# Kernel tuning notes

Hardware: AMD Instinct MI355X
Metric: run time of the kernel (lower is better)

The kernel has to match this reference:

```python
import jax, jax.numpy as jnp
import numpy as np


def _conv(x, w, b, stride, pad):
    y = jax.lax.conv_general_dilated(x, w, (stride, stride), [(pad, pad), (pad, pad)],
                                     dimension_numbers=('NCHW', 'OIHW', 'NCHW'))
    return y + b[None, :, None, None]


def _maxpool(x, k, s, pad=0):
    # PyTorch MaxPool2d pads with -inf
    return jax.lax.reduce_window(x, -jnp.inf, jax.lax.max,
                                 (1, 1, k, k), (1, 1, s, s),
                                 [(0, 0), (0, 0), (pad, pad), (pad, pad)])


def _squash(s):
    # squash along last axis: ||s||^2/(1+||s||^2) * s/||s||
    sq = jnp.sum(s * s, axis=-1, keepdims=True)
    return (sq / (1.0 + sq)) * s / jnp.sqrt(sq + 1e-8)


def setup_inputs() -> dict:
    key = jax.random.key(0)
    ks = jax.random.split(key, 16)

    def w(k, shape, fan_in):
        return jax.random.normal(k, shape, jnp.float32) / np.float32(np.sqrt(fan_in))

    inp = {}
    inp['x'] = jax.random.normal(ks[0], (64, 3, 227, 227), jnp.float32)
    # AlexNet conv stack
    inp['w1'] = w(ks[1], (96, 3, 11, 11), 3 * 11 * 11);   inp['b1'] = jnp.zeros((96,), jnp.float32)
    inp['w2'] = w(ks[2], (256, 96, 5, 5), 96 * 5 * 5);    inp['b2'] = jnp.zeros((256,), jnp.float32)
    inp['w3'] = w(ks[3], (384, 256, 3, 3), 256 * 3 * 3);  inp['b3'] = jnp.zeros((384,), jnp.float32)
    inp['w4'] = w(ks[4], (384, 384, 3, 3), 384 * 3 * 3);  inp['b4'] = jnp.zeros((384,), jnp.float32)
    inp['w5'] = w(ks[5], (256, 384, 3, 3), 384 * 3 * 3);  inp['b5'] = jnp.zeros((256,), jnp.float32)
    # PrimaryCaps: 32 caps * 8 dims = 256 output channels
    inp['pc_w'] = w(ks[6], (256, 256, 3, 3), 256 * 3 * 3); inp['pc_b'] = jnp.zeros((256,), jnp.float32)
    # DenseCapsule transform weights [out_caps, in_caps, out_dim, in_dim]
    inp['caps_W'] = 0.01 * jax.random.normal(ks[7], (101, 1152, 16, 8), jnp.float32)
    # MLP head (torch Linear convention: [out, in])
    inp['fc1_w'] = w(ks[8], (4096, 101 * 16), 101 * 16);  inp['fc1_b'] = jnp.zeros((4096,), jnp.float32)
    inp['fc2_w'] = w(ks[9], (4096, 4096), 4096);          inp['fc2_b'] = jnp.zeros((4096,), jnp.float32)
    inp['fc3_w'] = w(ks[10], (101, 4096), 4096);          inp['fc3_b'] = jnp.zeros((101,), jnp.float32)
    return inp


def reference(x, w1, b1, w2, b2, w3, b3, w4, b4, w5, b5,
              pc_w, pc_b, caps_W, fc1_w, fc1_b, fc2_w, fc2_b, fc3_w, fc3_b):
    # --- AlexNet conv stack ---
    h = jax.nn.relu(_conv(x, w1, b1, 4, 0))   # [B,96,55,55]
    h = _maxpool(h, 3, 2, 0)                   # [B,96,27,27]
    h = jax.nn.relu(_conv(h, w2, b2, 1, 2))    # [B,256,27,27]
    h = _maxpool(h, 3, 2, 1)                   # [B,256,14,14]
    h = jax.nn.relu(_conv(h, w3, b3, 1, 1))
    h = jax.nn.relu(_conv(h, w4, b4, 1, 1))
    h = jax.nn.relu(_conv(h, w5, b5, 1, 1))    # [B,256,14,14]
    h = _maxpool(h, 3, 2, 0)                   # [B,256,6,6]

    # --- PrimaryCaps: conv -> reshape to capsules -> squash ---
    p = _conv(h, pc_w, pc_b, 1, 1)             # [B,256,6,6]
    B = p.shape[0]
    u = _squash(p.reshape(B, -1, 8))           # [B,1152,8]

    # --- DenseCapsule dynamic routing (3 iterations) ---
    x_hat = jnp.einsum('jiod,bid->bjio', caps_W, u)   # [B,101,1152,16]
    x_hat_det = jax.lax.stop_gradient(x_hat)
    b_logits = jnp.zeros((B, 101, 1152), x_hat.dtype)
    routings = 3
    for r in range(routings):
        c = jax.nn.softmax(b_logits, axis=1)  # coupling coeffs over out caps
        if r == routings - 1:
            v = _squash(jnp.einsum('bji,bjio->bjo', c, x_hat))
        else:
            v = _squash(jnp.einsum('bji,bjio->bjo', c, x_hat_det))
            b_logits = b_logits + jnp.einsum('bjo,bjio->bji', v, x_hat_det)

    # --- MLP head (dropout in eval mode = identity) ---
    f = v.reshape(B, -1)                       # [B,1616]
    f = jax.nn.relu(f @ fc1_w.T + fc1_b)
    f = jax.nn.relu(f @ fc2_w.T + fc2_b)
    return f @ fc3_w.T + fc3_b                 # [B,101]
```

## Files before the change

kernel.cpp:

```cpp
#include <hip/hip_runtime.h>
#include <math.h>


#define BATCH 64
#define NJ 101
#define NI 1152
#define BJ (BATCH * NJ)
#define IC 64
#define NIC (NI / IC)
#define LDW 132

static inline int ceil_div(int a, int b) { return (a + b - 1) / b; }

typedef __attribute__((ext_vector_type(8))) short short8;
typedef __attribute__((ext_vector_type(4))) float f32x4;

__device__ __forceinline__ unsigned short f2bf(float f) {
    unsigned u = __float_as_uint(f);
    u += 0x7FFFu + ((u >> 16) & 1u);
    return (unsigned short)(u >> 16);
}
__device__ __forceinline__ float bf2f(unsigned short h) {
    return __uint_as_float(((unsigned)h) << 16);
}
__device__ __forceinline__ unsigned packsplit(float v) {
    unsigned short h = f2bf(v);
    unsigned short l = f2bf(v - bf2f(h));
    return ((unsigned)h << 16) | l;
}

__global__ void split_w(const float* __restrict__ w, unsigned short* __restrict__ hi,
                        unsigned short* __restrict__ lo, int Ktot, int Kp, int total) {
    int idx = blockIdx.x * 256 + threadIdx.x;
    if (idx >= total) return;
    int co = idx / Kp, kp = idx - co * Kp;
    float v = (kp < Ktot) ? w[(size_t)co * Ktot + kp] : 0.f;
    unsigned short h = f2bf(v);
    hi[idx] = h;
    lo[idx] = f2bf(v - bf2f(h));
}

template<int K, int STRIDE, int PAD, int WOUT, bool RELU, int TCO,
         bool INPK, bool OUTPK>
__global__ __launch_bounds__(256, 4) void conv_mfma(
        const void* __restrict__ inv, const float* __restrict__ wgt,
        const unsigned short* __restrict__ whi, const unsigned short* __restrict__ wlo,
        const float* __restrict__ bias, void* __restrict__ outv,
        int CIN, int COUT, int WIN, int Kp) {
    constexpr int KK  = K * K;
    constexpr int NSP = WOUT * WOUT;
    constexpr int LDH = 40;
    constexpr int NT  = TCO / 32;
    __shared__ unsigned short Ahs[TCO * LDH], Als[TCO * LDH];
    __shared__ unsigned short Bhs[64 * LDH],  Bls[64 * LDH];

    const int Ktot  = CIN * KK;
    const int WINSQ = WIN * WIN;

    const int tid  = threadIdx.x;
    const int px0  = blockIdx.x * 64;
    const int co0  = blockIdx.y * TCO;
    const int wave = tid >> 6;
    const int lane = tid & 63;
    const int ln15 = lane & 15;
    const int kq   = lane >> 4;
    const int coH  = (wave & 1) * (TCO / 2);
    const int pxH  = (wave >> 1) * 32;

    const int bpx = tid & 63;
    int p    = px0 + bpx;
    int bimg = p / NSP;
    int sp   = p - bimg * NSP;
    int ho   = sp / WOUT;
    int wo   = sp - ho * WOUT;
    const int hi0   = ho * STRIDE - PAD;
    const int wi0   = wo * STRIDE - PAD;
    const int bBase = bimg * CIN * WINSQ;

    const int aco = tid >> 3;
    const int ak4 = tid & 7;

    f32x4 acc[NT][2];
#pragma unroll
    for (int ct = 0; ct < NT; ++ct)
#pragma unroll
        for (int pt = 0; pt < 2; ++pt)
            acc[ct][pt] = (f32x4){0.f, 0.f, 0.f, 0.f};

    const int nchunks = (Ktot + 31) / 32;
    for (int c = 0; c < nchunks; ++c) {
        const int k0 = c * 32;
        if (whi) {
#pragma unroll
            for (int it = 0; it < TCO / 32; ++it) {
                int slot = tid + it * 256;
                int co = slot >> 3;
                int k4 = slot & 7;
                int row = (co0 + co) * Kp + k0 + k4 * 4;
                ushort4 h4 = *(const ushort4*)&whi[row];
                ushort4 l4 = *(const ushort4*)&wlo[row];
                *(ushort4*)&Ahs[co * LDH + k4 * 4] = h4;
                *(ushort4*)&Als[co * LDH + k4 * 4] = l4;
            }
        } else {
#pragma unroll
            for (int it = 0; it < TCO / 32; ++it) {
                int slot = tid + it * 256;
                int co = slot >> 3;
                int k4 = slot & 7;
                int k  = k0 + k4 * 4;
                float4 w4 = make_float4(0.f, 0.f, 0.f, 0.f);
                const float* wp = wgt + (size_t)(co0 + co) * Ktot + k;
                if (k + 3 < Ktot) {
                    w4 = *(const float4*)wp;
                } else {
                    if (k + 0 < Ktot) w4.x = wp[0];
                    if (k + 1 < Ktot) w4.y = wp[1];
                    if (k + 2 < Ktot) w4.z = wp[2];
                    if (k + 3 < Ktot) w4.w = wp[3];
                }
                unsigned short h0 = f2bf(w4.x), h1 = f2bf(w4.y),
                               h2 = f2bf(w4.z), h3 = f2bf(w4.w);
                unsigned short l0 = f2bf(w4.x - bf2f(h0)), l1 = f2bf(w4.y - bf2f(h1)),
                               l2 = f2bf(w4.z - bf2f(h2)), l3 = f2bf(w4.w - bf2f(h3));
                *(uint2*)&Ahs[co * LDH + k4 * 4] =
                    make_uint2(h0 | ((unsigned)h1 << 16), h2 | ((unsigned)h3 << 16));
                *(uint2*)&Als[co * LDH + k4 * 4] =
                    make_uint2(l0 | ((unsigned)l1 << 16), l2 | ((unsigned)l3 << 16));
            }
        }
#pragma unroll
        for (int it = 0; it < 4; ++it) {
            int kp = (tid >> 6) + it * 4;
            if (INPK) {
                const unsigned* inp = (const unsigned*)inv;
                unsigned u0 = 0, u1 = 0;
#pragma unroll
                for (int e = 0; e < 2; ++e) {
                    int k = k0 + kp * 2 + e;
                    unsigned v = 0;
                    if (k < Ktot) {
                        int ci = k / KK;
                        int r  = k - ci * KK;
                        int kh = r / K;
                        int kw = r - kh * K;
                        int hh = hi0 + kh;
                        int ww = wi0 + kw;
                        bool ok = true;
                        if (PAD > 0)
                            ok = ((unsigned)hh < (unsigned)WIN) &&
                                 ((unsigned)ww < (unsigned)WIN);
                        if (ok) v = inp[bBase + ci * WINSQ + hh * WIN + ww];
                    }
                    if (e == 0) u0 = v; else u1 = v;
                }
                *(unsigned*)&Bhs[bpx * LDH + kp * 2] = (u0 >> 16) | (u1 & 0xFFFF0000u);
                *(unsigned*)&Bls[bpx * LDH + kp * 2] = (u0 & 0xFFFFu) | (u1 << 16);
            } else {
                const float* inp = (const float*)inv;
                float f0 = 0.f, f1 = 0.f;
#pragma unroll
                for (int e = 0; e < 2; ++e) {
                    int k = k0 + kp * 2 + e;
                    float v = 0.f;
                    if (k < Ktot) {
                        int ci = k / KK;
                        int r  = k - ci * KK;
                        int kh = r / K;
                        int kw = r - kh * K;
                        int hh = hi0 + kh;
                        int ww = wi0 + kw;
                        bool ok = true;
                        if (PAD > 0)
                            ok = ((unsigned)hh < (unsigned)WIN) &&
                                 ((unsigned)ww < (unsigned)WIN);
                        if (ok) v = inp[bBase + ci * WINSQ + hh * WIN + ww];
                    }
                    if (e == 0) f0 = v; else f1 = v;
                }
                unsigned short h0 = f2bf(f0), h1 = f2bf(f1);
                unsigned short l0 = f2bf(f0 - bf2f(h0)), l1 = f2bf(f1 - bf2f(h1));
                *(unsigned*)&Bhs[bpx * LDH + kp * 2] = h0 | ((unsigned)h1 << 16);
                *(unsigned*)&Bls[bpx * LDH + kp * 2] = l0 | ((unsigned)l1 << 16);
            }
        }
        __syncthreads();

        short8 ahf[NT], alf[NT], bhf[2], blf[2];
#pragma unroll
        for (int ct = 0; ct < NT; ++ct) {
            int m = coH + ct * 16 + ln15;
            ahf[ct] = *(const short8*)&Ahs[m * LDH + kq * 8];
            alf[ct] = *(const short8*)&Als[m * LDH + kq * 8];
        }
#pragma unroll
        for (int pt = 0; pt < 2; ++pt) {
            int n = pxH + pt * 16 + ln15;
            bhf[pt] = *(const short8*)&Bhs[n * LDH + kq * 8];
            blf[pt] = *(const short8*)&Bls[n * LDH + kq * 8];
        }
#pragma unroll
        for (int ct = 0; ct < NT; ++ct)
#pragma unroll
            for (int pt = 0; pt < 2; ++pt) {
                acc[ct][pt] = __builtin_amdgcn_mfma_f32_16x16x32_bf16(
                    ahf[ct], bhf[pt], acc[ct][pt], 0, 0, 0);
                acc[ct][pt] = __builtin_amdgcn_mfma_f32_16x16x32_bf16(
                    ahf[ct], blf[pt], acc[ct][pt], 0, 0, 0);
                acc[ct][pt] = __builtin_amdgcn_mfma_f32_16x16x32_bf16(
                    alf[ct], bhf[pt], acc[ct][pt], 0, 0, 0);
            }
        __syncthreads();
    }

    float bv[NT][4];
#pragma unroll
    for (int ct = 0; ct < NT; ++ct)
#pragma unroll
        for (int r = 0; r < 4; ++r)
            bv[ct][r] = bias[co0 + coH + ct * 16 + kq * 4 + r];
#pragma unroll
    for (int pt = 0; pt < 2; ++pt) {
        int pg  = px0 + pxH + pt * 16 + ln15;
        int b2  = pg / NSP;
        int sp2 = pg - b2 * NSP;
#pragma unroll
        for (int ct = 0; ct < NT; ++ct) {
#pragma unroll
            for (int r = 0; r < 4; ++r) {
                int co = co0 + coH + ct * 16 + kq * 4 + r;
                float vv = acc[ct][pt][r] + bv[ct][r];
                if (RELU) vv = fmaxf(vv, 0.f);
                size_t oi = (size_t)(b2 * COUT + co) * NSP + sp2;
                if (OUTPK) ((unsigned*)outv)[oi] = packsplit(vv);
                else       ((float*)outv)[oi] = vv;
            }
        }
    }
}

__global__ void maxpool_pack(const float* __restrict__ in, unsigned* __restrict__ out,
                             int BC, int HIN, int WIN, int HOUT, int WOUT,
                             int KS, int S, int P) {
    int idx = blockIdx.x * blockDim.x + threadIdx.x;
    int total = BC * HOUT * WOUT;
    if (idx >= total) return;
    int wo = idx % WOUT;
    int ho = (idx / WOUT) % HOUT;
    int bc = idx / (WOUT * HOUT);
    int h0 = ho * S - P, w0 = wo * S - P;
    int h1 = h0 + KS, w1 = w0 + KS;
    if (h0 < 0) h0 = 0;
    if (w0 < 0) w0 = 0;
    if (h1 > HIN) h1 = HIN;
    if (w1 > WIN) w1 = WIN;
    const float* base = in + (size_t)bc * HIN * WIN;
    float m = -INFINITY;
    for (int h = h0; h < h1; h++)
        for (int w = w0; w < w1; w++)
            m = fmaxf(m, base[h * WIN + w]);
    out[idx] = packsplit(m);
}

__global__ void squash_u(const float* __restrict__ p, float* __restrict__ u, int ncaps) {
    int idx = blockIdx.x * blockDim.x + threadIdx.x;
    if (idx >= ncaps) return;
    const float4* pp = (const float4*)(p + (size_t)idx * 8);
    float4 a = pp[0], b = pp[1];
    float sq = a.x*a.x + a.y*a.y + a.z*a.z + a.w*a.w
             + b.x*b.x + b.y*b.y + b.z*b.z + b.w*b.w;
    float scale = (sq / (1.f + sq)) / sqrtf(sq + 1e-8f);
    float4* uu = (float4*)(u + (size_t)idx * 8);
    float4 oa, ob;
    oa.x = a.x*scale; oa.y = a.y*scale; oa.z = a.z*scale; oa.w = a.w*scale;
    ob.x = b.x*scale; ob.y = b.y*scale; ob.z = b.z*scale; ob.w = b.w*scale;
    uu[0] = oa; uu[1] = ob;
}

__global__ void softmax_j(const float* __restrict__ blog, float* __restrict__ c,
                          int Bn, int J, int I) {
    int idx = blockIdx.x * blockDim.x + threadIdx.x;
    if (idx >= Bn * I) return;
    int b = idx / I, i = idx - b * I;
    const float* base = blog + (size_t)b * J * I + i;
    float m = -INFINITY;
    for (int j = 0; j < J; j++) m = fmaxf(m, base[(size_t)j * I]);
    float* cb = c + (size_t)b * J * I + i;
    float sum = 0.f;
    for (int j = 0; j < J; j++) {
        float e = expf(base[(size_t)j * I] - m);
        sum += e;
        cb[(size_t)j * I] = e;
    }
    float inv = 1.f / sum;
    for (int j = 0; j < J; j++) cb[(size_t)j * I] *= inv;
}

__device__ __forceinline__ void stage_W(const float* __restrict__ W,
                                        float* __restrict__ wsh,
                                        int j, int i0, int tid) {
    const float4* Wp = (const float4*)(W + ((size_t)j * NI + i0) * 128);
#pragma unroll
    for (int p = 0; p < 8; ++p) {
        int vi  = p * 256 + tid;
        int row = vi >> 5;
        int c4  = vi & 31;
        float4 f = Wp[vi];
        *(float4*)&wsh[row * LDW + c4 * 4] = f;
    }
}

__global__ __launch_bounds__(256) void route_s_w(
        const float* __restrict__ c, const float* __restrict__ u,
        const float* __restrict__ W, float* __restrict__ ppart, int uniform) {
    __shared__ float wsh[IC * LDW];
    const int tid = threadIdx.x;
    const int icb = blockIdx.x;
    const int j   = blockIdx.y;
    const int i0  = icb * IC;

    stage_W(W, wsh, j, i0, tid);
    __syncthreads();

    const int bg = tid >> 4;
    const int iq = tid & 15;
    const float invJ = 1.f / (float)NJ;

    float s[4][16];
#pragma unroll
    for (int bb = 0; bb < 4; ++bb)
#pragma unroll
        for (int o = 0; o < 16; ++o) s[bb][o] = 0.f;

#pragma unroll
    for (int k = 0; k < 4; ++k) {
        int il = iq + 16 * k;
        int ig = i0 + il;
        const float* wr = &wsh[il * LDW];
        float4 ua[4], ub[4];
        float cc[4];
#pragma unroll
        for (int bb = 0; bb < 4; ++bb) {
            int b = bg * 4 + bb;
            const float4* up = (const float4*)(u + ((size_t)b * NI + ig) * 8);
            ua[bb] = up[0];
            ub[bb] = up[1];
            cc[bb] = uniform ? invJ : c[((size_t)b * NJ + j) * NI + ig];
        }
#pragma unroll
        for (int o = 0; o < 16; ++o) {
            float4 w0 = *(const float4*)&wr[o * 8];
            float4 w1 = *(const float4*)&wr[o * 8 + 4];
#pragma unroll
            for (int bb = 0; bb < 4; ++bb) {
                float dot = w0.x*ua[bb].x + w0.y*ua[bb].y + w0.z*ua[bb].z + w0.w*ua[bb].w
                          + w1.x*ub[bb].x + w1.y*ub[bb].y + w1.z*ub[bb].z + w1.w*ub[bb].w;
                s[bb][o] = fmaf(cc[bb], dot, s[bb][o]);
            }
        }
    }

#pragma unroll
    for (int off = 8; off > 0; off >>= 1)
#pragma unroll
        for (int bb = 0; bb < 4; ++bb)
#pragma unroll
            for (int o = 0; o < 16; ++o)
                s[bb][o] += __shfl_down(s[bb][o], off, 16);

    if (iq == 0) {
#pragma unroll
        for (int bb = 0; bb < 4; ++bb) {
            int b = bg * 4 + bb;
            size_t base = ((size_t)icb * BJ + (size_t)b * NJ + j) * 16;
#pragma unroll
            for (int o4 = 0; o4 < 4; ++o4)
                *(float4*)&ppart[base + o4 * 4] =
                    make_float4(s[bb][o4*4+0], s[bb][o4*4+1], s[bb][o4*4+2], s[bb][o4*4+3]);
        }
    }
}

__global__ __launch_bounds__(64) void reduce_squash(
        const float* __restrict__ ppart, float* __restrict__ v) {
    int l = threadIdx.x >> 4;
    int o = threadIdx.x & 15;
    int bj = blockIdx.x * 4 + l;
    float s = 0.f;
    for (int ic = 0; ic < NIC; ic++)
        s += ppart[((size_t)ic * BJ + bj) * 16 + o];
    __shared__ float sarr[4][16];
    sarr[l][o] = s;
    __syncthreads();
    float ssq = 0.f;
#pragma unroll
    for (int k = 0; k < 16; k++) { float t = sarr[l][k]; ssq += t * t; }
    float scale = (ssq / (1.f + ssq)) / sqrtf(ssq + 1e-8f);
    v[(size_t)bj * 16 + o] = s * scale;
}

__global__ __launch_bounds__(256) void route_bupd_w(
        const float* __restrict__ u, const float* __restrict__ W,
        const float* __restrict__ v, float* __restrict__ blog, int accumulate) {
    __shared__ float wsh[IC * LDW];
    const int tid = threadIdx.x;
    const int icb = blockIdx.x;
    const int j   = blockIdx.y;
    const int i0  = icb * IC;

    stage_W(W, wsh, j, i0, tid);
    __syncthreads();

    const int bg = tid >> 4;
    const int iq = tid & 15;

    float vv[4][16];
#pragma unroll
    for (int bb = 0; bb < 4; ++bb) {
        int b = bg * 4 + bb;
        const float4* vp = (const float4*)(v + ((size_t)b * NJ + j) * 16);
#pragma unroll
        for (int o4 = 0; o4 < 4; ++o4) {
            float4 f = vp[o4];
            vv[bb][o4*4+0] = f.x; vv[bb][o4*4+1] = f.y;
            vv[bb][o4*4+2] = f.z; vv[bb][o4*4+3] = f.w;
        }
    }

#pragma unroll
    for (int k = 0; k < 4; ++k) {
        int il = iq + 16 * k;
        int ig = i0 + il;
        const float* wr = &wsh[il * LDW];
        float4 ua[4], ub[4];
#pragma unroll
        for (int bb = 0; bb < 4; ++bb) {
            int b = bg * 4 + bb;
            const float4* up = (const float4*)(u + ((size_t)b * NI + ig) * 8);
            ua[bb] = up[0];
            ub[bb] = up[1];
        }
        float acc[4] = {0.f, 0.f, 0.f, 0.f};
#pragma unroll
        for (int o = 0; o < 16; ++o) {
            float4 w0 = *(const float4*)&wr[o * 8];
            float4 w1 = *(const float4*)&wr[o * 8 + 4];
#pragma unroll
            for (int bb = 0; bb < 4; ++bb) {
                float dot = w0.x*ua[bb].x + w0.y*ua[bb].y + w0.z*ua[bb].z + w0.w*ua[bb].w
                          + w1.x*ub[bb].x + w1.y*ub[bb].y + w1.z*ub[bb].z + w1.w*ub[bb].w;
                acc[bb] = fmaf(vv[bb][o], dot, acc[bb]);
            }
        }
#pragma unroll
        for (int bb = 0; bb < 4; ++bb) {
            int b = bg * 4 + bb;
            size_t idx = ((size_t)b * NJ + j) * NI + ig;
            blog[idx] = accumulate ? (blog[idx] + acc[bb]) : acc[bb];
        }
    }
}

template<bool RELU>
__global__ __launch_bounds__(256, 4) void fc_gemm(
        const float* __restrict__ in, const float* __restrict__ w,
        const float* __restrict__ bias, float* __restrict__ out,
        int M, int N, int Kd) {
    constexpr int KC  = 32;
    constexpr int LDA = 68;
    __shared__ float Ash[KC * LDA];
    __shared__ float Bsh[KC * LDA];

    const int tid = threadIdx.x;
    const int n0 = blockIdx.x * 64;

    const int tn = tid & 15;
    const int tm = tid >> 4;

    float acc[4][4] = {{0.f}};

    for (int k0 = 0; k0 < Kd; k0 += KC) {
#pragma unroll
        for (int it = 0; it < 2; ++it) {
            int idx = tid + it * 256;
            int n   = idx >> 3;
            int k4  = idx & 7;
            int k   = k0 + k4 * 4;
            float4 w4 = make_float4(0.f, 0.f, 0.f, 0.f);
            int ng = n0 + n;
            if (ng < N) {
                const float* wp = w + (size_t)ng * Kd + k;
                if (k + 3 < Kd) {
                    w4 = *(const float4*)wp;
                } else {
                    if (k + 0 < Kd) w4.x = wp[0];
                    if (k + 1 < Kd) w4.y = wp[1];
                    if (k + 2 < Kd) w4.z = wp[2];
                    if (k + 3 < Kd) w4.w = wp[3];
                }
            }
            Ash[(k4 * 4 + 0) * LDA + n] = w4.x;
            Ash[(k4 * 4 + 1) * LDA + n] = w4.y;
            Ash[(k4 * 4 + 2) * LDA + n] = w4.z;
            Ash[(k4 * 4 + 3) * LDA + n] = w4.w;
        }
#pragma unroll
        for (int it = 0; it < 2; ++it) {
            int idx = tid + it * 256;
            int m   = idx >> 3;
            int k4  = idx & 7;
            int k   = k0 + k4 * 4;
            float4 x4 = make_float4(0.f, 0.f, 0.f, 0.f);
            if (m < M) {
                const float* xp = in + (size_t)m * Kd + k;
                if (k + 3 < Kd) {
                    x4 = *(const float4*)xp;
                } else {
                    if (k + 0 < Kd) x4.x = xp[0];
                    if (k + 1 < Kd) x4.y = xp[1];
                    if (k + 2 < Kd) x4.z = xp[2];
                    if (k + 3 < Kd) x4.w = xp[3];
                }
            }
            Bsh[(k4 * 4 + 0) * LDA + m] = x4.x;
            Bsh[(k4 * 4 + 1) * LDA + m] = x4.y;
            Bsh[(k4 * 4 + 2) * LDA + m] = x4.z;
            Bsh[(k4 * 4 + 3) * LDA + m] = x4.w;
        }
        __syncthreads();
#pragma unroll
        for (int kk = 0; kk < KC; ++kk) {
            float4 a4 = *(const float4*)&Ash[kk * LDA + tn * 4];
            float4 b4 = *(const float4*)&Bsh[kk * LDA + tm * 4];
            float av[4] = {a4.x, a4.y, a4.z, a4.w};
            float bv[4] = {b4.x, b4.y, b4.z, b4.w};
#pragma unroll
            for (int i = 0; i < 4; ++i)
#pragma unroll
                for (int j = 0; j < 4; ++j)
                    acc[i][j] = fmaf(av[i], bv[j], acc[i][j]);
        }
        __syncthreads();
    }

#pragma unroll
    for (int i = 0; i < 4; ++i) {
        int ng = n0 + tn * 4 + i;
        if (ng >= N) continue;
        float bs = bias[ng];
#pragma unroll
        for (int j = 0; j < 4; ++j) {
            int m = tm * 4 + j;
            if (m >= M) continue;
            float vv = acc[i][j] + bs;
            if (RELU) vv = fmaxf(vv, 0.f);
            out[(size_t)m * N + ng] = vv;
        }
    }
}

extern "C" void kernel_launch(void* const* d_in, const int* in_sizes, int n_in,
                              void* d_out, int out_size, void* d_ws, size_t ws_size,
                              hipStream_t stream) {
    const float* x     = (const float*)d_in[0];
    const float* w1    = (const float*)d_in[1];
    const float* b1    = (const float*)d_in[2];
    const float* w2    = (const float*)d_in[3];
    const float* b2    = (const float*)d_in[4];
    const float* w3    = (const float*)d_in[5];
    const float* b3    = (const float*)d_in[6];
    const float* w4    = (const float*)d_in[7];
    const float* b4    = (const float*)d_in[8];
    const float* w5    = (const float*)d_in[9];
    const float* b5    = (const float*)d_in[10];
    const float* pc_w  = (const float*)d_in[11];
    const float* pc_b  = (const float*)d_in[12];
    const float* capsW = (const float*)d_in[13];
    const float* fc1_w = (const float*)d_in[14];
    const float* fc1_b = (const float*)d_in[15];
    const float* fc2_w = (const float*)d_in[16];
    const float* fc2_b = (const float*)d_in[17];
    const float* fc3_w = (const float*)d_in[18];
    const float* fc3_b = (const float*)d_in[19];
    float* outp = (float*)d_out;

    char* ws = (char*)d_ws;
    float* A  = (float*)ws;
    float* Bb = (float*)(ws + ((size_t)80 << 20));
    float* Dd = (float*)(ws + ((size_t)100 << 20));
    float* blog  = A;
    float* csm   = A + 7446528;
    float* ppart = A + 2 * 7446528;
    float* vcap = Dd;
    float* f1   = Dd + 131072;
    float* f2   = Dd + 131072 + 262144;

    const size_t WPL_ELEMS = 2ull * (96*384 + 256*2400 + 384*2304 +
                                     384*3456 + 256*3456 + 256*2304);
    const size_t WPL_NEED  = ((size_t)104 << 20) + WPL_ELEMS * 2;
    const bool wsplit = ws_size >= WPL_NEED;
    unsigned short* wp = (unsigned short*)(ws + ((size_t)104 << 20));
    unsigned short *w1h=nullptr,*w1l=nullptr,*w2h=nullptr,*w2l=nullptr,
                   *w3h=nullptr,*w3l=nullptr,*w4h=nullptr,*w4l=nullptr,
                   *w5h=nullptr,*w5l=nullptr,*pch=nullptr,*pcl=nullptr;
    if (wsplit) {
        size_t off = 0;
        auto alloc2 = [&](size_t n, unsigned short** h, unsigned short** l) {
            *h = wp + off; *l = wp + off + n; off += 2 * n;
        };
        alloc2((size_t)96*384,  &w1h, &w1l);
        alloc2((size_t)256*2400, &w2h, &w2l);
        alloc2((size_t)384*2304, &w3h, &w3l);
        alloc2((size_t)384*3456, &w4h, &w4l);
        alloc2((size_t)256*3456, &w5h, &w5l);
        alloc2((size_t)256*2304, &pch, &pcl);
        split_w<<<dim3(ceil_div(96*384, 256)), dim3(256), 0, stream>>>(
            w1, w1h, w1l, 363, 384, 96*384);
        split_w<<<dim3(ceil_div(256*2400, 256)), dim3(256), 0, stream>>>(
            w2, w2h, w2l, 2400, 2400, 256*2400);
        split_w<<<dim3(ceil_div(384*2304, 256)), dim3(256), 0, stream>>>(
            w3, w3h, w3l, 2304, 2304, 384*2304);
        split_w<<<dim3(ceil_div(384*3456, 256)), dim3(256), 0, stream>>>(
            w4, w4h, w4l, 3456, 3456, 384*3456);
        split_w<<<dim3(ceil_div(256*3456, 256)), dim3(256), 0, stream>>>(
            w5, w5h, w5l, 3456, 3456, 256*3456);
        split_w<<<dim3(ceil_div(256*2304, 256)), dim3(256), 0, stream>>>(
            pc_w, pch, pcl, 2304, 2304, 256*2304);
    }

    const int B = BATCH;

    conv_mfma<11, 4, 0, 55, true, 96, false, false>
        <<<dim3(3025, 1), dim3(256), 0, stream>>>(
        x, w1, w1h, w1l, b1, A, 3, 96, 227, 384);
    maxpool_pack<<<dim3(ceil_div(B * 96 * 27 * 27, 256)), dim3(256), 0, stream>>>(
        A, (unsigned*)Bb, B * 96, 55, 55, 27, 27, 3, 2, 0);
    conv_mfma<5, 1, 2, 27, true, 128, true, false>
        <<<dim3(729, 2), dim3(256), 0, stream>>>(
        Bb, w2, w2h, w2l, b2, A, 96, 256, 27, 2400);
    maxpool_pack<<<dim3(ceil_div(B * 256 * 14 * 14, 256)), dim3(256), 0, stream>>>(
        A, (unsigned*)Bb, B * 256, 27, 27, 14, 14, 3, 2, 1);
    conv_mfma<3, 1, 1, 14, true, 128, true, true>
        <<<dim3(196, 3), dim3(256), 0, stream>>>(
        Bb, w3, w3h, w3l, b3, A, 256, 384, 14, 2304);
    conv_mfma<3, 1, 1, 14, true, 128, true, true>
        <<<dim3(196, 3), dim3(256), 0, stream>>>(
        A, w4, w4h, w4l, b4, Bb, 384, 384, 14, 3456);
    conv_mfma<3, 1, 1, 14, true, 128, true, false>
        <<<dim3(196, 2), dim3(256), 0, stream>>>(
        Bb, w5, w5h, w5l, b5, A, 384, 256, 14, 3456);
    maxpool_pack<<<dim3(ceil_div(B * 256 * 6 * 6, 256)), dim3(256), 0, stream>>>(
        A, (unsigned*)Bb, B * 256, 14, 14, 6, 6, 3, 2, 0);
    conv_mfma<3, 1, 1, 6, false, 64, true, false>
        <<<dim3(36, 4), dim3(256), 0, stream>>>(
        Bb, pc_w, pch, pcl, pc_b, A, 256, 256, 6, 2304);
    squash_u<<<dim3(ceil_div(B * 1152, 256)), dim3(256), 0, stream>>>(A, Bb, B * 1152);

    dim3 rgrid(NIC, NJ);
    route_s_w<<<rgrid, dim3(256), 0, stream>>>(csm, Bb, capsW, ppart, 1);
    reduce_squash<<<dim3(BJ / 4), dim3(64), 0, stream>>>(ppart, vcap);
    route_bupd_w<<<rgrid, dim3(256), 0, stream>>>(Bb, capsW, vcap, blog, 0);
    softmax_j<<<dim3(ceil_div(B * NI, 256)), dim3(256), 0, stream>>>(
        blog, csm, B, NJ, NI);
    route_s_w<<<rgrid, dim3(256), 0, stream>>>(csm, Bb, capsW, ppart, 0);
    reduce_squash<<<dim3(BJ / 4), dim3(64), 0, stream>>>(ppart, vcap);
    route_bupd_w<<<rgrid, dim3(256), 0, stream>>>(Bb, capsW, vcap, blog, 1);
    softmax_j<<<dim3(ceil_div(B * NI, 256)), dim3(256), 0, stream>>>(
        blog, csm, B, NJ, NI);
    route_s_w<<<rgrid, dim3(256), 0, stream>>>(csm, Bb, capsW, ppart, 0);
    reduce_squash<<<dim3(BJ / 4), dim3(64), 0, stream>>>(ppart, vcap);

    fc_gemm<true><<<dim3(64), dim3(256), 0, stream>>>(vcap, fc1_w, fc1_b, f1, B, 4096, 1616);
    fc_gemm<true><<<dim3(64), dim3(256), 0, stream>>>(f1, fc2_w, fc2_b, f2, B, 4096, 4096);
    fc_gemm<false><<<dim3(2), dim3(256), 0, stream>>>(f2, fc3_w, fc3_b, outp, B, 101, 4096);
}
```

Baseline: 3.485 ms.

## Prefetch next conv K-chunk into registers and swizzle B tile in LDS

The conv MFMA kernel now gathers the next 32-wide K chunk of weights and im2col inputs into registers while the current chunk's MFMAs run, then stores them to LDS at the top of the next iteration. The B tile columns are XOR-swizzled by pixel index to cut LDS bank conflicts on the stores and on the short8 fragment reads. This hides global-load latency behind compute, at the cost of more registers per thread, which could lower occupancy under the launch bounds of 256 threads and 4 blocks.

```diff
diff --git a/kernel.cpp b/kernel.cpp
--- a/kernel.cpp
+++ b/kernel.cpp
@@ -28,6 +28,7 @@
     unsigned short l = f2bf(v - bf2f(h));
     return ((unsigned)h << 16) | l;
 }
+__device__ __forceinline__ int bswz(int n) { return ((n >> 2) ^ (n >> 4)) & 3; }
 
 __global__ void split_w(const float* __restrict__ w, unsigned short* __restrict__ hi,
                         unsigned short* __restrict__ lo, int Ktot, int Kp, int total) {
@@ -51,6 +52,7 @@
     constexpr int NSP = WOUT * WOUT;
     constexpr int LDH = 40;
     constexpr int NT  = TCO / 32;
+    constexpr int NTA = TCO / 32;
     __shared__ unsigned short Ahs[TCO * LDH], Als[TCO * LDH];
     __shared__ unsigned short Bhs[64 * LDH],  Bls[64 * LDH];
 
@@ -76,6 +78,8 @@
     const int hi0   = ho * STRIDE - PAD;
     const int wi0   = wo * STRIDE - PAD;
     const int bBase = bimg * CIN * WINSQ;
+    const int swzb  = bswz(bpx);
+    const int wq    = tid >> 6;
 
     const int aco = tid >> 3;
     const int ak4 = tid & 7;
@@ -87,24 +91,23 @@
         for (int pt = 0; pt < 2; ++pt)
             acc[ct][pt] = (f32x4){0.f, 0.f, 0.f, 0.f};
 
-    const int nchunks = (Ktot + 31) / 32;
-    for (int c = 0; c < nchunks; ++c) {
-        const int k0 = c * 32;
+    ushort4 pah[NTA], pal[NTA];
+    uint2 pb_cur[4], pb_nxt[4];
+
+    auto gatherA = [&](int k0) {
         if (whi) {
 #pragma unroll
-            for (int it = 0; it < TCO / 32; ++it) {
+            for (int it = 0; it < NTA; ++it) {
                 int slot = tid + it * 256;
                 int co = slot >> 3;
                 int k4 = slot & 7;
                 int row = (co0 + co) * Kp + k0 + k4 * 4;
-                ushort4 h4 = *(const ushort4*)&whi[row];
-                ushort4 l4 = *(const ushort4*)&wlo[row];
-                *(ushort4*)&Ahs[co * LDH + k4 * 4] = h4;
-                *(ushort4*)&Als[co * LDH + k4 * 4] = l4;
+                pah[it] = *(const ushort4*)&whi[row];
+                pal[it] = *(const ushort4*)&wlo[row];
             }
         } else {
 #pragma unroll
-            for (int it = 0; it < TCO / 32; ++it) {
+            for (int it = 0; it < NTA; ++it) {
                 int slot = tid + it * 256;
                 int co = slot >> 3;
                 int k4 = slot & 7;
@@ -121,17 +124,17 @@
                 }
                 unsigned short h0 = f2bf(w4.x), h1 = f2bf(w4.y),
                                h2 = f2bf(w4.z), h3 = f2bf(w4.w);
-                unsigned short l0 = f2bf(w4.x - bf2f(h0)), l1 = f2bf(w4.y - bf2f(h1)),
-                               l2 = f2bf(w4.z - bf2f(h2)), l3 = f2bf(w4.w - bf2f(h3));
-                *(uint2*)&Ahs[co * LDH + k4 * 4] =
-                    make_uint2(h0 | ((unsigned)h1 << 16), h2 | ((unsigned)h3 << 16));
-                *(uint2*)&Als[co * LDH + k4 * 4] =
-                    make_uint2(l0 | ((unsigned)l1 << 16), l2 | ((unsigned)l3 << 16));
-            }
-        }
+                pah[it] = make_ushort4(h0, h1, h2, h3);
+                pal[it] = make_ushort4(f2bf(w4.x - bf2f(h0)), f2bf(w4.y - bf2f(h1)),
+                                       f2bf(w4.z - bf2f(h2)), f2bf(w4.w - bf2f(h3)));
+            }
+        }
+    };
+
+    auto gatherB = [&](int k0, uint2* pb) {
 #pragma unroll
         for (int it = 0; it < 4; ++it) {
-            int kp = (tid >> 6) + it * 4;
+            int kp = wq + it * 4;
             if (INPK) {
                 const unsigned* inp = (const unsigned*)inv;
                 unsigned u0 = 0, u1 = 0;
@@ -154,8 +157,8 @@
                     }
                     if (e == 0) u0 = v; else u1 = v;
                 }
-                *(unsigned*)&Bhs[bpx * LDH + kp * 2] = (u0 >> 16) | (u1 & 0xFFFF0000u);
-                *(unsigned*)&Bls[bpx * LDH + kp * 2] = (u0 & 0xFFFFu) | (u1 << 16);
+                pb[it].x = (u0 >> 16) | (u1 & 0xFFFF0000u);
+                pb[it].y = (u0 & 0xFFFFu) | (u1 << 16);
             } else {
                 const float* inp = (const float*)inv;
                 float f0 = 0.f, f1 = 0.f;
@@ -179,12 +182,38 @@
                     if (e == 0) f0 = v; else f1 = v;
                 }
                 unsigned short h0 = f2bf(f0), h1 = f2bf(f1);
-                unsigned short l0 = f2bf(f0 - bf2f(h0)), l1 = f2bf(f1 - bf2f(h1));
-                *(unsigned*)&Bhs[bpx * LDH + kp * 2] = h0 | ((unsigned)h1 << 16);
-                *(unsigned*)&Bls[bpx * LDH + kp * 2] = l0 | ((unsigned)l1 << 16);
-            }
+                pb[it].x = h0 | ((unsigned)h1 << 16);
+                pb[it].y = (unsigned)f2bf(f0 - bf2f(h0)) |
+                           ((unsigned)f2bf(f1 - bf2f(h1)) << 16);
+            }
+        }
+    };
+
+    const int nchunks = (Ktot + 31) / 32;
+    gatherA(0);
+    gatherB(0, pb_cur);
+
+    for (int c = 0; c < nchunks; ++c) {
+#pragma unroll
+        for (int it = 0; it < NTA; ++it) {
+            int slot = tid + it * 256;
+            int co = slot >> 3;
+            int k4 = slot & 7;
+            *(ushort4*)&Ahs[co * LDH + k4 * 4] = pah[it];
+            *(ushort4*)&Als[co * LDH + k4 * 4] = pal[it];
+        }
+#pragma unroll
+        for (int it = 0; it < 4; ++it) {
+            int colh = ((it ^ swzb) << 3) + (wq << 1);
+            *(unsigned*)&Bhs[bpx * LDH + colh] = pb_cur[it].x;
+            *(unsigned*)&Bls[bpx * LDH + colh] = pb_cur[it].y;
         }
         __syncthreads();
+
+        if (c + 1 < nchunks) {
+            gatherA((c + 1) * 32);
+            gatherB((c + 1) * 32, pb_nxt);
+        }
 
         short8 ahf[NT], alf[NT], bhf[2], blf[2];
 #pragma unroll
@@ -196,8 +225,9 @@
 #pragma unroll
         for (int pt = 0; pt < 2; ++pt) {
             int n = pxH + pt * 16 + ln15;
-            bhf[pt] = *(const short8*)&Bhs[n * LDH + kq * 8];
-            blf[pt] = *(const short8*)&Bls[n * LDH + kq * 8];
+            int oct = kq ^ bswz(n);
+            bhf[pt] = *(const short8*)&Bhs[n * LDH + oct * 8];
+            blf[pt] = *(const short8*)&Bls[n * LDH + oct * 8];
         }
 #pragma unroll
         for (int ct = 0; ct < NT; ++ct)
@@ -211,6 +241,11 @@
                     alf[ct], bhf[pt], acc[ct][pt], 0, 0, 0);
             }
         __syncthreads();
+
+        if (c + 1 < nchunks) {
+#pragma unroll
+            for (int it = 0; it < 4; ++it) pb_cur[it] = pb_nxt[it];
+        }
     }
 
     float bv[NT][4];
```

New measurement: 3.623 ms. 1.04x slower.

## Reorder conv reduction to kernel-position outer loop with transposed split weights

Applied to the files above, without the earlier changes.

Adds a conv kernel variant for conv2–conv5 and PrimaryCaps that loops over kernel positions outside and 32-channel chunks inside. The per-element im2col index decode (div/mod by K*K and K) and per-element bounds checks are replaced by one bounds check per kernel position. Weights are pre-split into a [kpos][chunk][cout][32] layout so each tile loads contiguously. This assumes CIN is a multiple of 32, and the wasted halo padding on small layers is unchanged.

```diff
diff --git a/kernel.cpp b/kernel.cpp
--- a/kernel.cpp
+++ b/kernel.cpp
@@ -40,9 +40,27 @@
     lo[idx] = f2bf(v - bf2f(h));
 }
 
+__global__ void split_w_t(const float* __restrict__ w, unsigned short* __restrict__ hi,
+                          unsigned short* __restrict__ lo, int CIN, int KKv,
+                          int COUT, int total) {
+    int idx = blockIdx.x * 256 + threadIdx.x;
+    if (idx >= total) return;
+    int kk = idx & 31;
+    int r  = idx >> 5;
+    int co = r % COUT;
+    int r2 = r / COUT;
+    int nCC  = CIN >> 5;
+    int cc   = r2 % nCC;
+    int kpos = r2 / nCC;
+    float v = w[((size_t)co * CIN + cc * 32 + kk) * KKv + kpos];
+    unsigned short h = f2bf(v);
+    hi[idx] = h;
+    lo[idx] = f2bf(v - bf2f(h));
+}
+
 template<int K, int STRIDE, int PAD, int WOUT, bool RELU, int TCO,
          bool INPK, bool OUTPK>
-__global__ __launch_bounds__(256, 4) void conv_mfma(
+__global__ __launch_bounds__(256, 4) void conv_mfma_g(
         const void* __restrict__ inv, const float* __restrict__ wgt,
         const unsigned short* __restrict__ whi, const unsigned short* __restrict__ wlo,
         const float* __restrict__ bias, void* __restrict__ outv,
@@ -77,9 +95,6 @@
     const int wi0   = wo * STRIDE - PAD;
     const int bBase = bimg * CIN * WINSQ;
 
-    const int aco = tid >> 3;
-    const int ak4 = tid & 7;
-
     f32x4 acc[NT][2];
 #pragma unroll
     for (int ct = 0; ct < NT; ++ct)
@@ -97,10 +112,8 @@
                 int co = slot >> 3;
                 int k4 = slot & 7;
                 int row = (co0 + co) * Kp + k0 + k4 * 4;
-                ushort4 h4 = *(const ushort4*)&whi[row];
-                ushort4 l4 = *(const ushort4*)&wlo[row];
-                *(ushort4*)&Ahs[co * LDH + k4 * 4] = h4;
-                *(ushort4*)&Als[co * LDH + k4 * 4] = l4;
+                *(ushort4*)&Ahs[co * LDH + k4 * 4] = *(const ushort4*)&whi[row];
+                *(ushort4*)&Als[co * LDH + k4 * 4] = *(const ushort4*)&wlo[row];
             }
         } else {
 #pragma unroll
@@ -121,12 +134,10 @@
                 }
                 unsigned short h0 = f2bf(w4.x), h1 = f2bf(w4.y),
                                h2 = f2bf(w4.z), h3 = f2bf(w4.w);
-                unsigned short l0 = f2bf(w4.x - bf2f(h0)), l1 = f2bf(w4.y - bf2f(h1)),
-                               l2 = f2bf(w4.z - bf2f(h2)), l3 = f2bf(w4.w - bf2f(h3));
-                *(uint2*)&Ahs[co * LDH + k4 * 4] =
-                    make_uint2(h0 | ((unsigned)h1 << 16), h2 | ((unsigned)h3 << 16));
-                *(uint2*)&Als[co * LDH + k4 * 4] =
-                    make_uint2(l0 | ((unsigned)l1 << 16), l2 | ((unsigned)l3 << 16));
+                *(ushort4*)&Ahs[co * LDH + k4 * 4] = make_ushort4(h0, h1, h2, h3);
+                *(ushort4*)&Als[co * LDH + k4 * 4] =
+                    make_ushort4(f2bf(w4.x - bf2f(h0)), f2bf(w4.y - bf2f(h1)),
+                                 f2bf(w4.z - bf2f(h2)), f2bf(w4.w - bf2f(h3)));
             }
         }
 #pragma unroll
@@ -179,9 +190,10 @@
                     if (e == 0) f0 = v; else f1 = v;
                 }
                 unsigned short h0 = f2bf(f0), h1 = f2bf(f1);
-                unsigned short l0 = f2bf(f0 - bf2f(h0)), l1 = f2bf(f1 - bf2f(h1));
                 *(unsigned*)&Bhs[bpx * LDH + kp * 2] = h0 | ((unsigned)h1 << 16);
-                *(unsigned*)&Bls[bpx * LDH + kp * 2] = l0 | ((unsigned)l1 << 16);
+                *(unsigned*)&Bls[bpx * LDH + kp * 2] =
+                    (unsigned)f2bf(f0 - bf2f(h0)) |
+                    ((unsigned)f2bf(f1 - bf2f(h1)) << 16);
             }
         }
         __syncthreads();
@@ -211,6 +223,180 @@
                     alf[ct], bhf[pt], acc[ct][pt], 0, 0, 0);
             }
         __syncthreads();
+    }
+
+    float bv[NT][4];
+#pragma unroll
+    for (int ct = 0; ct < NT; ++ct)
+#pragma unroll
+        for (int r = 0; r < 4; ++r)
+            bv[ct][r] = bias[co0 + coH + ct * 16 + kq * 4 + r];
+#pragma unroll
+    for (int pt = 0; pt < 2; ++pt) {
+        int pg  = px0 + pxH + pt * 16 + ln15;
+        int b2  = pg / NSP;
+        int sp2 = pg - b2 * NSP;
+#pragma unroll
+        for (int ct = 0; ct < NT; ++ct) {
+#pragma unroll
+            for (int r = 0; r < 4; ++r) {
+                int co = co0 + coH + ct * 16 + kq * 4 + r;
+                float vv = acc[ct][pt][r] + bv[ct][r];
+                if (RELU) vv = fmaxf(vv, 0.f);
+                size_t oi = (size_t)(b2 * COUT + co) * NSP + sp2;
+                if (OUTPK) ((unsigned*)outv)[oi] = packsplit(vv);
+                else       ((float*)outv)[oi] = vv;
+            }
+        }
+    }
+}
+
+template<int K, int STRIDE, int PAD, int WOUT, bool RELU, int TCO,
+         bool INPK, bool OUTPK>
+__global__ __launch_bounds__(256, 4) void conv_mfma_k(
+        const void* __restrict__ inv, const float* __restrict__ wgt,
+        const unsigned short* __restrict__ whi, const unsigned short* __restrict__ wlo,
+        const float* __restrict__ bias, void* __restrict__ outv,
+        int CIN, int COUT, int WIN) {
+    constexpr int KK  = K * K;
+    constexpr int NSP = WOUT * WOUT;
+    constexpr int LDH = 40;
+    constexpr int NT  = TCO / 32;
+    __shared__ unsigned short Ahs[TCO * LDH], Als[TCO * LDH];
+    __shared__ unsigned short Bhs[64 * LDH],  Bls[64 * LDH];
+
+    const int WINSQ = WIN * WIN;
+    const int nCC   = CIN >> 5;
+
+    const int tid  = threadIdx.x;
+    const int px0  = blockIdx.x * 64;
+    const int co0  = blockIdx.y * TCO;
+    const int wave = tid >> 6;
+    const int lane = tid & 63;
+    const int ln15 = lane & 15;
+    const int kq   = lane >> 4;
+    const int coH  = (wave & 1) * (TCO / 2);
+    const int pxH  = (wave >> 1) * 32;
+
+    const int bpx = tid & 63;
+    int p    = px0 + bpx;
+    int bimg = p / NSP;
+    int sp   = p - bimg * NSP;
+    int ho   = sp / WOUT;
+    int wo   = sp - ho * WOUT;
+    const int hi0   = ho * STRIDE - PAD;
+    const int wi0   = wo * STRIDE - PAD;
+    const int bBase = bimg * CIN * WINSQ;
+    const int wq    = tid >> 6;
+
+    f32x4 acc[NT][2];
+#pragma unroll
+    for (int ct = 0; ct < NT; ++ct)
+#pragma unroll
+        for (int pt = 0; pt < 2; ++pt)
+            acc[ct][pt] = (f32x4){0.f, 0.f, 0.f, 0.f};
+
+#pragma unroll 1
+    for (int kpos = 0; kpos < KK; ++kpos) {
+        const int kh = kpos / K;
+        const int kw = kpos - kh * K;
+        const int hh = hi0 + kh;
+        const int ww = wi0 + kw;
+        bool ok = true;
+        if (PAD > 0)
+            ok = ((unsigned)hh < (unsigned)WIN) && ((unsigned)ww < (unsigned)WIN);
+        const int pbase = bBase + hh * WIN + ww;
+
+        for (int cc = 0; cc < nCC; ++cc) {
+            if (whi) {
+                const size_t wrow = (((size_t)kpos * nCC + cc) * COUT) << 5;
+#pragma unroll
+                for (int it = 0; it < TCO / 32; ++it) {
+                    int slot = tid + it * 256;
+                    int co = slot >> 3;
+                    int k4 = slot & 7;
+                    size_t idx = wrow + (((size_t)(co0 + co)) << 5) + k4 * 4;
+                    *(ushort4*)&Ahs[co * LDH + k4 * 4] = *(const ushort4*)&whi[idx];
+                    *(ushort4*)&Als[co * LDH + k4 * 4] = *(const ushort4*)&wlo[idx];
+                }
+            } else {
+#pragma unroll
+                for (int it = 0; it < TCO / 32; ++it) {
+                    int slot = tid + it * 256;
+                    int co = slot >> 3;
+                    int k4 = slot & 7;
+                    unsigned short h[4], l[4];
+#pragma unroll
+                    for (int j = 0; j < 4; ++j) {
+                        int ci = cc * 32 + k4 * 4 + j;
+                        float v = wgt[((size_t)(co0 + co) * CIN + ci) * KK + kpos];
+                        h[j] = f2bf(v);
+                        l[j] = f2bf(v - bf2f(h[j]));
+                    }
+                    *(ushort4*)&Ahs[co * LDH + k4 * 4] =
+                        make_ushort4(h[0], h[1], h[2], h[3]);
+                    *(ushort4*)&Als[co * LDH + k4 * 4] =
+                        make_ushort4(l[0], l[1], l[2], l[3]);
+                }
+            }
+#pragma unroll
+            for (int it = 0; it < 4; ++it) {
+                int kp  = wq + it * 4;
+                int ci0 = cc * 32 + kp * 2;
+                int a0  = pbase + ci0 * WINSQ;
+                if (INPK) {
+                    const unsigned* inp = (const unsigned*)inv;
+                    unsigned u0 = 0, u1 = 0;
+                    if (ok) {
+                        u0 = inp[a0];
+                        u1 = inp[a0 + WINSQ];
+                    }
+                    *(unsigned*)&Bhs[bpx * LDH + kp * 2] =
+                        (u0 >> 16) | (u1 & 0xFFFF0000u);
+                    *(unsigned*)&Bls[bpx * LDH + kp * 2] =
+                        (u0 & 0xFFFFu) | (u1 << 16);
+                } else {
+                    const float* inp = (const float*)inv;
+                    float f0 = 0.f, f1 = 0.f;
+                    if (ok) {
+                        f0 = inp[a0];
+                        f1 = inp[a0 + WINSQ];
+                    }
+                    unsigned short h0 = f2bf(f0), h1 = f2bf(f1);
+                    *(unsigned*)&Bhs[bpx * LDH + kp * 2] = h0 | ((unsigned)h1 << 16);
+                    *(unsigned*)&Bls[bpx * LDH + kp * 2] =
+                        (unsigned)f2bf(f0 - bf2f(h0)) |
+                        ((unsigned)f2bf(f1 - bf2f(h1)) << 16);
+                }
+            }
+            __syncthreads();
+
+            short8 ahf[NT], alf[NT], bhf[2], blf[2];
+#pragma unroll
+            for (int ct = 0; ct < NT; ++ct) {
+                int m = coH + ct * 16 + ln15;
+                ahf[ct] = *(const short8*)&Ahs[m * LDH + kq * 8];
+                alf[ct] = *(const short8*)&Als[m * LDH + kq * 8];
+            }
+#pragma unroll
+            for (int pt = 0; pt < 2; ++pt) {
+                int n = pxH + pt * 16 + ln15;
+                bhf[pt] = *(const short8*)&Bhs[n * LDH + kq * 8];
+                blf[pt] = *(const short8*)&Bls[n * LDH + kq * 8];
+            }
+#pragma unroll
+            for (int ct = 0; ct < NT; ++ct)
+#pragma unroll
+                for (int pt = 0; pt < 2; ++pt) {
+                    acc[ct][pt] = __builtin_amdgcn_mfma_f32_16x16x32_bf16(
+                        ahf[ct], bhf[pt], acc[ct][pt], 0, 0, 0);
+                    acc[ct][pt] = __builtin_amdgcn_mfma_f32_16x16x32_bf16(
+                        ahf[ct], blf[pt], acc[ct][pt], 0, 0, 0);
+                    acc[ct][pt] = __builtin_amdgcn_mfma_f32_16x16x32_bf16(
+                        alf[ct], bhf[pt], acc[ct][pt], 0, 0, 0);
+                }
+            __syncthreads();
+        }
     }
 
     float bv[NT][4];
@@ -595,8 +781,13 @@
     float* f1   = Dd + 131072;
     float* f2   = Dd + 131072 + 262144;
 
-    const size_t WPL_ELEMS = 2ull * (96*384 + 256*2400 + 384*2304 +
-                                     384*3456 + 256*3456 + 256*2304);
+    const size_t N1 = (size_t)96 * 384;
+    const size_t N2 = (size_t)25 * 96 * 256;
+    const size_t N3 = (size_t)9 * 256 * 384;
+    const size_t N4 = (size_t)9 * 384 * 384;
+    const size_t N5 = (size_t)9 * 384 * 256;
+    const size_t NP = (size_t)9 * 256 * 256;
+    const size_t WPL_ELEMS = 2 * (N1 + N2 + N3 + N4 + N5 + NP);
     const size_t WPL_NEED  = ((size_t)104 << 20) + WPL_ELEMS * 2;
     const bool wsplit = ws_size >= WPL_NEED;
     unsigned short* wp = (unsigned short*)(ws + ((size_t)104 << 20));
@@ -608,52 +799,52 @@
         auto alloc2 = [&](size_t n, unsigned short** h, unsigned short** l) {
             *h = wp + off; *l = wp + off + n; off += 2 * n;
         };
-        alloc2((size_t)96*384,  &w1h, &w1l);
-        alloc2((size_t)256*2400, &w2h, &w2l);
-        alloc2((size_t)384*2304, &w3h, &w3l);
-        alloc2((size_t)384*3456, &w4h, &w4l);
-        alloc2((size_t)256*3456, &w5h, &w5l);
-        alloc2((size_t)256*2304, &pch, &pcl);
-        split_w<<<dim3(ceil_div(96*384, 256)), dim3(256), 0, stream>>>(
-            w1, w1h, w1l, 363, 384, 96*384);
-        split_w<<<dim3(ceil_div(256*2400, 256)), dim3(256), 0, stream>>>(
-            w2, w2h, w2l, 2400, 2400, 256*2400);
-        split_w<<<dim3(ceil_div(384*2304, 256)), dim3(256), 0, stream>>>(
-            w3, w3h, w3l, 2304, 2304, 384*2304);
-        split_w<<<dim3(ceil_div(384*3456, 256)), dim3(256), 0, stream>>>(
-            w4, w4h, w4l, 3456, 3456, 384*3456);
-        split_w<<<dim3(ceil_div(256*3456, 256)), dim3(256), 0, stream>>>(
-            w5, w5h, w5l, 3456, 3456, 256*3456);
-        split_w<<<dim3(ceil_div(256*2304, 256)), dim3(256), 0, stream>>>(
-            pc_w, pch, pcl, 2304, 2304, 256*2304);
+        alloc2(N1, &w1h, &w1l);
+        alloc2(N2, &w2h, &w2l);
+        alloc2(N3, &w3h, &w3l);
+        alloc2(N4, &w4h, &w4l);
+        alloc2(N5, &w5h, &w5l);
+        alloc2(NP, &pch, &pcl);
+        split_w<<<dim3(ceil_div((int)N1, 256)), dim3(256), 0, stream>>>(
+            w1, w1h, w1l, 363, 384, (int)N1);
+        split_w_t<<<dim3(ceil_div((int)N2, 256)), dim3(256), 0, stream>>>(
+            w2, w2h, w2l, 96, 25, 256, (int)N2);
+        split_w_t<<<dim3(ceil_div((int)N3, 256)), dim3(256), 0, stream>>>(
+            w3, w3h, w3l, 256, 9, 384, (int)N3);
+        split_w_t<<<dim3(ceil_div((int)N4, 256)), dim3(256), 0, stream>>>(
+            w4, w4h, w4l, 384, 9, 384, (int)N4);
+        split_w_t<<<dim3(ceil_div((int)N5, 256)), dim3(256), 0, stream>>>(
+            w5, w5h, w5l, 384, 9, 256, (int)N5);
+        split_w_t<<<dim3(ceil_div((int)NP, 256)), dim3(256), 0, stream>>>(
+            pc_w, pch, pcl, 256, 9, 256, (int)NP);
     }
 
     const int B = BATCH;
 
-    conv_mfma<11, 4, 0, 55, true, 96, false, false>
+    conv_mfma_g<11, 4, 0, 55, true, 96, false, false>
         <<<dim3(3025, 1), dim3(256), 0, stream>>>(
         x, w1, w1h, w1l, b1, A, 3, 96, 227, 384);
     maxpool_pack<<<dim3(ceil_div(B * 96 * 27 * 27, 256)), dim3(256), 0, stream>>>(
         A, (unsigned*)Bb, B * 96, 55, 55, 27, 27, 3, 2, 0);
-    conv_mfma<5, 1, 2, 27, true, 128, true, false>
+    conv_mfma_k<5, 1, 2, 27, true, 128, true, false>
         <<<dim3(729, 2), dim3(256), 0, stream>>>(
-        Bb, w2, w2h, w2l, b2, A, 96, 256, 27, 2400);
+        Bb, w2, w2h, w2l, b2, A, 96, 256, 27);
     maxpool_pack<<<dim3(ceil_div(B * 256 * 14 * 14, 256)), dim3(256), 0, stream>>>(
         A, (unsigned*)Bb, B * 256, 27, 27, 14, 14, 3, 2, 1);
-    conv_mfma<3, 1, 1, 14, true, 128, true, true>
+    conv_mfma_k<3, 1, 1, 14, true, 128, true, true>
         <<<dim3(196, 3), dim3(256), 0, stream>>>(
-        Bb, w3, w3h, w3l, b3, A, 256, 384, 14, 2304);
-    conv_mfma<3, 1, 1, 14, true, 128, true, true>
+        Bb, w3, w3h, w3l, b3, A, 256, 384, 14);
+    conv_mfma_k<3, 1, 1, 14, true, 128, true, true>
         <<<dim3(196, 3), dim3(256), 0, stream>>>(
-        A, w4, w4h, w4l, b4, Bb, 384, 384, 14, 3456);
-    conv_mfma<3, 1, 1, 14, true, 128, true, false>
+        A, w4, w4h, w4l, b4, Bb, 384, 384, 14);
+    conv_mfma_k<3, 1, 1, 14, true, 128, true, false>
         <<<dim3(196, 2), dim3(256), 0, stream>>>(
-        Bb, w5, w5h, w5l, b5, A, 384, 256, 14, 3456);
+        Bb, w5, w5h, w5l, b5, A, 384, 256, 14);
     maxpool_pack<<<dim3(ceil_div(B * 256 * 6 * 6, 256)), dim3(256), 0, stream>>>(
         A, (unsigned*)Bb, B * 256, 14, 14, 6, 6, 3, 2, 0);
-    conv_mfma<3, 1, 1, 6, false, 64, true, false>
+    conv_mfma_k<3, 1, 1, 6, false, 64, true, false>
         <<<dim3(36, 4), dim3(256), 0, stream>>>(
-        Bb, pc_w, pch, pcl, pc_b, A, 256, 256, 6, 2304);
+        Bb, pc_w, pch, pcl, pc_b, A, 256, 256, 6);
     squash_u<<<dim3(ceil_div(B * 1152, 256)), dim3(256), 0, stream>>>(A, Bb, B * 1152);
 
     dim3 rgrid(NIC, NJ);
```

Measured after the change: 3.777 ms. +8.4%, slower.
